# Performance work log

Measured on AMD Instinct MI355X. Metric: run time of the kernel, lower is better.

## Reference

```python
import jax, jax.numpy as jnp
import numpy as np

B, N, F, D, DEG, LAYERS = 32, 1024, 64, 128, 8, 3
EPS = 1e-5


def _gat(x, src, dst, mask, W, a_s, a_d, b):
    # PyG GATConv (heads=1, concat=True): remove existing self loops (handled by mask),
    # add one self loop per node, per-edge leaky-relu attention, scatter-softmax per target.
    M = x.shape[0]
    h = x @ W                                 # [M, D]
    es = h @ a_s                              # [M] source attention term (x*att_src).sum(-1)
    ed = h @ a_d                              # [M] target attention term
    sl = jnp.arange(M, dtype=src.dtype)
    s = jnp.concatenate([src, sl])
    d = jnp.concatenate([dst, sl])
    m = jnp.concatenate([mask, jnp.ones((M,), bool)])
    logit = jnp.where(m, jax.nn.leaky_relu(es[s] + ed[d], 0.2), -jnp.inf)
    mx = jax.ops.segment_max(logit, d, num_segments=M)  # finite: every node has a self loop
    ex = jnp.where(m, jnp.exp(logit - mx[d]), 0.0)
    den = jax.ops.segment_sum(ex, d, num_segments=M)
    alpha = ex / den[d]
    return jax.ops.segment_sum(alpha[:, None] * h[s], d, num_segments=M) + b


def _dedupe(src, dst, mask, M):
    # coalesce after pooling: drop self loops and duplicate edges (PyG max_pool/pool_edge)
    E = src.shape[0]
    key = src * M + dst
    key = jnp.where(mask, key, M * M + jnp.arange(E, dtype=key.dtype))  # park dead edges on unique keys
    order = jnp.argsort(key)
    sk = key[order]
    first = jnp.concatenate([jnp.ones((1,), bool), sk[1:] != sk[:-1]])
    uniq = jnp.zeros((E,), bool).at[order].set(first)
    return mask & uniq & (src != dst)


def _forward(x, Ws, att_src, att_dst, bias, edge_index, clusters):
    src, dst = edge_index[0], edge_index[1]
    mask = src != dst  # GATConv calls remove_self_loops before adding its own
    Bn = x.shape[0] // clusters[0].shape[0]
    for i in range(len(Ws)):
        x = jax.nn.relu(_gat(x, src, dst, mask, Ws[i], att_src[i], att_dst[i], bias[i]))
        c = clusters[i]
        Ni = c.shape[0]
        No = Ni // 2  # cluster maps are arange(Ni)//2, surjective onto Ni//2
        cl = jnp.tile(c, Bn) + jnp.repeat(jnp.arange(Bn, dtype=c.dtype) * No, Ni)
        x = jax.ops.segment_max(x, cl, num_segments=Bn * No)  # max_pool over clusters
        src, dst = cl[src], cl[dst]
        mask = _dedupe(src, dst, mask, Bn * No)
        mu = jnp.mean(x, axis=0)  # BatchNorm1d(affine=False), training-mode batch stats
        var = jnp.mean((x - mu) ** 2, axis=0)
        x = (x - mu) / jnp.sqrt(var + EPS)
    return x.reshape(Bn, -1)  # [B, final_node * dim_cell]


def setup_inputs() -> dict:
    key = jax.random.key(0)
    ks = jax.random.split(key, 10)
    x = jax.random.normal(ks[0], (B * N, F), jnp.float32)
    # per-graph random edges with per-graph node offsets (graph-major layout)
    src_l = jax.random.randint(ks[1], (B, N * DEG), 0, N)
    dst_l = jax.random.randint(ks[2], (B, N * DEG), 0, N)
    off = (jnp.arange(B) * N)[:, None]
    edge_index = jnp.stack([(src_l + off).reshape(-1), (dst_l + off).reshape(-1)]).astype(jnp.int32)
    c0 = (jnp.arange(N) // 2).astype(jnp.int32)
    c1 = (jnp.arange(N // 2) // 2).astype(jnp.int32)
    c2 = (jnp.arange(N // 4) // 2).astype(jnp.int32)
    W0 = jax.random.normal(ks[3], (F, D), jnp.float32) / np.float32(np.sqrt(F))
    W1 = jax.random.normal(ks[4], (D, D), jnp.float32) / np.float32(np.sqrt(D))
    W2 = jax.random.normal(ks[5], (D, D), jnp.float32) / np.float32(np.sqrt(D))
    att_src = jax.random.normal(ks[6], (LAYERS, D), jnp.float32) / np.float32(np.sqrt(D))
    att_dst = jax.random.normal(ks[7], (LAYERS, D), jnp.float32) / np.float32(np.sqrt(D))
    bias = jnp.zeros((LAYERS, D), jnp.float32)
    return dict(x=x, W0=W0, W1=W1, W2=W2, att_src=att_src, att_dst=att_dst, bias=bias,
                edge_index=edge_index, c0=c0, c1=c1, c2=c2)


def reference(x, W0, W1, W2, att_src, att_dst, bias, edge_index, c0, c1, c2):
    return _forward(x, [W0, W1, W2], att_src, att_dst, bias, edge_index, [c0, c1, c2])
```

## Files before the change

### kernel.cpp

```cpp
#include <hip/hip_runtime.h>

#define E_TOTAL 262144
#define NGRAPH  32
#define EPG     8192
#define EPS_BN  1e-5f
#define MB (1u << 20)
#define KB (1u << 10)

__device__ __forceinline__ float lrelu(float x){ return x > 0.f ? x : 0.2f * x; }

__device__ __forceinline__ int xcd_swz(int b, int n){ return (b & 7) * (n >> 3) + (b >> 3); }

template<int Q>
__device__ __forceinline__ void scan_bins(int* h, int* cnt_g, int* rs_g, int B, int g,
                                          int ebase, int* wsum){
  int t = threadIdx.x, lane = t & 63, w = t >> 6;
  int c[Q]; int s = 0;
  #pragma unroll
  for (int i = 0; i < Q; ++i){ c[i] = h[t * Q + i]; s += c[i]; }
  int v = s;
  #pragma unroll
  for (int o = 1; o < 64; o <<= 1){ int u = __shfl_up(v, o); if (lane >= o) v += u; }
  if (lane == 63) wsum[w] = v;
  __syncthreads();
  if (t == 0){ int run = 0;
    #pragma unroll
    for (int i = 0; i < 4; ++i){ int x = wsum[i]; wsum[i] = run; run += x; } }
  __syncthreads();
  int run = v - s + wsum[w];
  #pragma unroll
  for (int i = 0; i < Q; ++i){
    cnt_g[g * B + t * Q + i] = c[i];
    rs_g [g * B + t * Q + i] = ebase + run;
    h[t * Q + i] = run;
    run += c[i];
  }
  __syncthreads();
}

__global__ __launch_bounds__(256, 2)
void mega1(const float* __restrict__ x0, const float* __restrict__ W0,
           const float* __restrict__ a_s, const float* __restrict__ a_d,
           const int* __restrict__ src0, const int* __restrict__ dst0,
           float* __restrict__ C, float* __restrict__ es, float* __restrict__ ed,
           int* __restrict__ csr1, int* __restrict__ csr2, int* __restrict__ csr3,
           int* __restrict__ rs1, int* __restrict__ rs2, int* __restrict__ rs3,
           int* __restrict__ cnt1, int* __restrict__ cnt2, int* __restrict__ cnt3,
           float* __restrict__ partials_all){
  __shared__ __align__(16) char smem[45072];
  __shared__ int wsum[4];
  int t = threadIdx.x;
  int raw = blockIdx.x;

  if (raw < 96){
    int* bm2 = (int*)smem;
    int* bm3 = bm2 + 8192;
    int* h   = bm3 + 2048;
    int role = raw >> 5, g = raw & 31, ebase = g * EPG;

    if (role == 0){
      for (int i = g * 256 + t; i < 3 * 64 * 256; i += 8192) partials_all[i] = 0.f;
      for (int i = t; i < 1024; i += 256) h[i] = 0;
      __syncthreads();
      for (int i = 0; i < 32; ++i){
        int e = ebase + i * 256 + t;
        int sv = src0[e], dv = dst0[e];
        if (sv != dv) atomicAdd(&h[dv & 1023], 1);
      }
      __syncthreads();
      scan_bins<4>(h, cnt1, rs1, 1024, g, ebase, wsum);
      for (int i = 0; i < 32; ++i){
        int e = ebase + i * 256 + t;
        int sv = src0[e], dv = dst0[e];
        if (sv != dv){
          int p = atomicAdd(&h[dv & 1023], 1);
          csr1[ebase + p] = sv;
        }
      }
    } else if (role == 1){
      for (int i = t; i < 8192; i += 256) bm2[i] = 0;
      for (int i = t; i < 512; i += 256) h[i] = 0;
      __syncthreads();
      unsigned int k2m = 0;
      for (int i = 0; i < 32; ++i){
        int e = ebase + i * 256 + t;
        int sv = src0[e], dv = dst0[e];
        if (sv != dv){
          int s2 = (sv >> 1) & 511, d2 = (dv >> 1) & 511;
          if (s2 != d2){
            int key = (s2 << 9) | d2;
            unsigned int bit = 1u << (key & 31);
            unsigned int old = atomicOr((unsigned int*)&bm2[key >> 5], bit);
            if (!(old & bit)){ k2m |= 1u << i; atomicAdd(&h[d2], 1); }
          }
        }
      }
      __syncthreads();
      scan_bins<2>(h, cnt2, rs2, 512, g, ebase, wsum);
      for (int i = 0; i < 32; ++i){
        if ((k2m >> i) & 1u){
          int e = ebase + i * 256 + t;
          int sv = src0[e], dv = dst0[e];
          int p = atomicAdd(&h[(dv >> 1) & 511], 1);
          csr2[ebase + p] = sv >> 1;
        }
      }
    } else {
      for (int i = t; i < 8192; i += 256) bm2[i] = 0;
      for (int i = t; i < 2048; i += 256) bm3[i] = 0;
      for (int i = t; i < 256; i += 256) h[i] = 0;
      __syncthreads();
      unsigned int k3m = 0;
      for (int i = 0; i < 32; ++i){
        int e = ebase + i * 256 + t;
        int sv = src0[e], dv = dst0[e];
        if (sv != dv){
          int s2 = (sv >> 1) & 511, d2 = (dv >> 1) & 511;
          if (s2 != d2){
            int key = (s2 << 9) | d2;
            unsigned int bit = 1u << (key & 31);
            unsigned int old = atomicOr((unsigned int*)&bm2[key >> 5], bit);
            if (!(old & bit)){
              int s3 = (sv >> 2) & 255, d3 = (dv >> 2) & 255;
              if (s3 != d3){
                int key3 = (s3 << 8) | d3;
                unsigned int b3 = 1u << (key3 & 31);
                unsigned int o3 = atomicOr((unsigned int*)&bm3[key3 >> 5], b3);
                if (!(o3 & b3)){ k3m |= 1u << i; atomicAdd(&h[d3], 1); }
              }
            }
          }
        }
      }
      __syncthreads();
      scan_bins<1>(h, cnt3, rs3, 256, g, ebase, wsum);
      for (int i = 0; i < 32; ++i){
        if ((k3m >> i) & 1u){
          int e = ebase + i * 256 + t;
          int sv = src0[e], dv = dst0[e];
          int p = atomicAdd(&h[(dv >> 2) & 255], 1);
          csr3[ebase + p] = sv >> 2;
        }
      }
    }
    return;
  }

  float* Ws   = (float*)smem;
  float* As_t = Ws + 8192;
  int tile = xcd_swz(raw - 96, 1024);
  int row0 = tile * 32;
  int c2 = t & 63, rg = t >> 6;
  float2 acc[8];
  #pragma unroll
  for (int i = 0; i < 8; ++i){ acc[i].x = 0.f; acc[i].y = 0.f; }

  for (int i = t; i < 8192; i += 256) Ws[i] = W0[i];
  #pragma unroll
  for (int it = 0; it < 8; ++it){
    int i = it * 256 + t;
    int r = i >> 6, kk = i & 63;
    As_t[kk * 36 + r] = x0[(size_t)(row0 + r) * 64 + kk];
  }
  __syncthreads();
  #pragma unroll 8
  for (int kk = 0; kk < 64; ++kk){
    float2 w = *(float2*)&Ws[kk * 128 + c2 * 2];
    float4 a0 = *(float4*)&As_t[kk * 36 + rg * 8];
    float4 a1 = *(float4*)&As_t[kk * 36 + rg * 8 + 4];
    acc[0].x = fmaf(a0.x, w.x, acc[0].x); acc[0].y = fmaf(a0.x, w.y, acc[0].y);
    acc[1].x = fmaf(a0.y, w.x, acc[1].x); acc[1].y = fmaf(a0.y, w.y, acc[1].y);
    acc[2].x = fmaf(a0.z, w.x, acc[2].x); acc[2].y = fmaf(a0.z, w.y, acc[2].y);
    acc[3].x = fmaf(a0.w, w.x, acc[3].x); acc[3].y = fmaf(a0.w, w.y, acc[3].y);
    acc[4].x = fmaf(a1.x, w.x, acc[4].x); acc[4].y = fmaf(a1.x, w.y, acc[4].y);
    acc[5].x = fmaf(a1.y, w.x, acc[5].x); acc[5].y = fmaf(a1.y, w.y, acc[5].y);
    acc[6].x = fmaf(a1.z, w.x, acc[6].x); acc[6].y = fmaf(a1.z, w.y, acc[6].y);
    acc[7].x = fmaf(a1.w, w.x, acc[7].x); acc[7].y = fmaf(a1.w, w.y, acc[7].y);
  }
  float2 as2 = ((const float2*)a_s)[c2];
  float2 ad2 = ((const float2*)a_d)[c2];
  float2* C2 = (float2*)C;
  #pragma unroll
  for (int i = 0; i < 8; ++i){
    int r = row0 + rg * 8 + i;
    C2[(size_t)r * 64 + c2] = acc[i];
    float e1 = acc[i].x * as2.x + acc[i].y * as2.y;
    float e2 = acc[i].x * ad2.x + acc[i].y * ad2.y;
    #pragma unroll
    for (int o = 32; o; o >>= 1){ e1 += __shfl_xor(e1, o); e2 += __shfl_xor(e2, o); }
    if (c2 == 0){ es[r] = e1; ed[r] = e2; }
  }
}

__global__ __launch_bounds__(256)
void gemm_attn128(const float* __restrict__ A, const float* __restrict__ W,
                  const float* __restrict__ partials, float invM,
                  const float* __restrict__ a_s, const float* __restrict__ a_d,
                  float* __restrict__ C, float* __restrict__ es, float* __restrict__ ed){
  __shared__ float Ws[64 * 128];
  __shared__ float As_t[64 * 36];
  __shared__ float red[256];
  __shared__ float bnmu[128], bnrs[128];
  int t = threadIdx.x;
  {
    float s = 0.f;
    #pragma unroll
    for (int k = 0; k < 64; ++k) s += partials[(k << 8) + t];
    red[t] = s;
  }
  __syncthreads();
  if (t < 128){
    float mu = red[t] * invM;
    float var = red[128 + t] * invM - mu * mu;
    bnmu[t] = mu; bnrs[t] = rsqrtf(var + EPS_BN);
  }
  int bid = xcd_swz(blockIdx.x, gridDim.x);
  int row0 = bid * 32;
  int c2 = t & 63, rg = t >> 6;
  float2 acc[8];
  #pragma unroll
  for (int i = 0; i < 8; ++i){ acc[i].x = 0.f; acc[i].y = 0.f; }

  for (int k0 = 0; k0 < 128; k0 += 64){
    __syncthreads();
    for (int i = t; i < 64 * 128; i += 256)
      Ws[i] = W[(size_t)(k0 + (i >> 7)) * 128 + (i & 127)];
    #pragma unroll
    for (int it = 0; it < 8; ++it){
      int i = it * 256 + t;
      int r = i >> 6, kk = i & 63;
      float v = A[(size_t)(row0 + r) * 128 + k0 + kk];
      v = (v - bnmu[k0 + kk]) * bnrs[k0 + kk];
      As_t[kk * 36 + r] = v;
    }
    __syncthreads();
    #pragma unroll 8
    for (int kk = 0; kk < 64; ++kk){
      float2 w = *(float2*)&Ws[kk * 128 + c2 * 2];
      float4 a0 = *(float4*)&As_t[kk * 36 + rg * 8];
      float4 a1 = *(float4*)&As_t[kk * 36 + rg * 8 + 4];
      acc[0].x = fmaf(a0.x, w.x, acc[0].x); acc[0].y = fmaf(a0.x, w.y, acc[0].y);
      acc[1].x = fmaf(a0.y, w.x, acc[1].x); acc[1].y = fmaf(a0.y, w.y, acc[1].y);
      acc[2].x = fmaf(a0.z, w.x, acc[2].x); acc[2].y = fmaf(a0.z, w.y, acc[2].y);
      acc[3].x = fmaf(a0.w, w.x, acc[3].x); acc[3].y = fmaf(a0.w, w.y, acc[3].y);
      acc[4].x = fmaf(a1.x, w.x, acc[4].x); acc[4].y = fmaf(a1.x, w.y, acc[4].y);
      acc[5].x = fmaf(a1.y, w.x, acc[5].x); acc[5].y = fmaf(a1.y, w.y, acc[5].y);
      acc[6].x = fmaf(a1.z, w.x, acc[6].x); acc[6].y = fmaf(a1.z, w.y, acc[6].y);
      acc[7].x = fmaf(a1.w, w.x, acc[7].x); acc[7].y = fmaf(a1.w, w.y, acc[7].y);
    }
  }
  float2 as2 = ((const float2*)a_s)[c2];
  float2 ad2 = ((const float2*)a_d)[c2];
  float2* C2 = (float2*)C;
  #pragma unroll
  for (int i = 0; i < 8; ++i){
    int r = row0 + rg * 8 + i;
    C2[(size_t)r * 64 + c2] = acc[i];
    float e1 = acc[i].x * as2.x + acc[i].y * as2.y;
    float e2 = acc[i].x * ad2.x + acc[i].y * ad2.y;
    #pragma unroll
    for (int o = 32; o; o >>= 1){ e1 += __shfl_xor(e1, o); e2 += __shfl_xor(e2, o); }
    if (c2 == 0){ es[r] = e1; ed[r] = e2; }
  }
}

__global__ void gat_pool(const float* __restrict__ h, const float* __restrict__ es,
                         const float* __restrict__ ed, const int* __restrict__ csr_src,
                         const int* __restrict__ row_start, const int* __restrict__ row_cnt,
                         const float* __restrict__ bias, float* __restrict__ xout,
                         float* __restrict__ partials, int M){
  __shared__ float2 osh[4][64];
  int lane = threadIdx.x & 63;
  int wave = threadIdx.x >> 6;
  int bid = xcd_swz(blockIdx.x, gridDim.x);
  int n = bid * 4 + wave;
  int start = row_start[n];
  int cnt   = row_cnt[n];
  float edn = ed[n];
  float selfl = lrelu(es[n] + edn);

  float m_l = -1e30f, d_l = 0.f;
  int   s_c = 0; float l_c = 0.f;
  for (int c0 = 0; c0 < cnt; c0 += 64){
    int j = c0 + lane;
    if (j < cnt){
      int s = csr_src[start + j];
      float l = lrelu(es[s] + edn);
      if (c0 == 0){ s_c = s; l_c = l; }
      float mn = fmaxf(m_l, l);
      d_l = d_l * __expf(m_l - mn) + __expf(l - mn);
      m_l = mn;
    }
  }
  #pragma unroll
  for (int o = 32; o; o >>= 1){
    float m2 = __shfl_xor(m_l, o), d2 = __shfl_xor(d_l, o);
    float mn = fmaxf(m_l, m2);
    d_l = d_l * __expf(m_l - mn) + d2 * __expf(m2 - mn);
    m_l = mn;
  }
  float mf  = fmaxf(m_l, selfl);
  float den = d_l * __expf(m_l - mf) + __expf(selfl - mf);

  const float2* h2 = (const float2*)h;
  float sw = __expf(selfl - mf);
  float2 hv = h2[(size_t)n * 64 + lane];
  float2 acc; acc.x = sw * hv.x; acc.y = sw * hv.y;
  for (int c0 = 0; c0 < cnt; c0 += 64){
    int j = c0 + lane;
    int s_j; float w_j;
    if (c0 == 0){
      s_j = s_c;
      w_j = (lane < cnt) ? __expf(l_c - mf) : 0.f;
    } else {
      s_j = 0; w_j = 0.f;
      if (j < cnt){
        s_j = csr_src[start + j];
        w_j = __expf(lrelu(es[s_j] + edn) - mf);
      }
    }
    int rem = min(64, cnt - c0);
    int k = 0;
    for (; k + 8 <= rem; k += 8){
      int ss[8]; float ww[8]; float2 hh[8];
      #pragma unroll
      for (int i = 0; i < 8; ++i){ ss[i] = __shfl(s_j, k + i); ww[i] = __shfl(w_j, k + i); }
      #pragma unroll
      for (int i = 0; i < 8; ++i){ hh[i] = h2[(size_t)ss[i] * 64 + lane]; }
      #pragma unroll
      for (int i = 0; i < 8; ++i){
        acc.x = fmaf(ww[i], hh[i].x, acc.x);
        acc.y = fmaf(ww[i], hh[i].y, acc.y);
      }
    }
    for (; k < rem; ++k){
      int s = __shfl(s_j, k); float w = __shfl(w_j, k);
      float2 hh = h2[(size_t)s * 64 + lane];
      acc.x = fmaf(w, hh.x, acc.x);
      acc.y = fmaf(w, hh.y, acc.y);
    }
  }
  float inv = 1.f / den;
  float2 bv = ((const float2*)bias)[lane];
  float2 o2;
  o2.x = fmaxf(acc.x * inv + bv.x, 0.f);
  o2.y = fmaxf(acc.y * inv + bv.y, 0.f);
  osh[wave][lane] = o2;
  __syncthreads();
  float2 p;
  if (wave < 2){
    float2 a = osh[2 * wave][lane], b = osh[2 * wave + 1][lane];
    p.x = fmaxf(a.x, b.x); p.y = fmaxf(a.y, b.y);
    ((float2*)xout)[(size_t)(bid * 2 + wave) * 64 + lane] = p;
  }
  __syncthreads();
  if (wave < 2) osh[wave][lane] = p;
  __syncthreads();
  float* part = partials + ((bid & 63) << 8);
  if (wave == 0){
    float2 a = osh[0][lane], b = osh[1][lane];
    atomicAdd(&part[2 * lane],     a.x + b.x);
    atomicAdd(&part[2 * lane + 1], a.y + b.y);
  } else if (wave == 1){
    float2 a = osh[0][lane], b = osh[1][lane];
    atomicAdd(&part[128 + 2 * lane],     a.x * a.x + b.x * b.x);
    atomicAdd(&part[128 + 2 * lane + 1], a.y * a.y + b.y * b.y);
  }
}

__global__ __launch_bounds__(256)
void bn_norm(const float* __restrict__ in, const float* __restrict__ partials,
             float* __restrict__ out, int M){
  __shared__ float red[256];
  __shared__ float mu_s[128], rs_s[128];
  int t = threadIdx.x;
  {
    float s = 0.f;
    #pragma unroll
    for (int k = 0; k < 64; ++k) s += partials[(k << 8) + t];
    red[t] = s;
  }
  __syncthreads();
  if (t < 128){
    float mu = red[t] / (float)M;
    float var = red[128 + t] / (float)M - mu * mu;
    mu_s[t] = mu; rs_s[t] = rsqrtf(var + EPS_BN);
  }
  __syncthreads();
  int total = M * 128;
  for (int idx = blockIdx.x * 256 + t; idx < total; idx += gridDim.x * 256){
    int c = idx & 127;
    out[idx] = (in[idx] - mu_s[c]) * rs_s[c];
  }
}

extern "C" void kernel_launch(void* const* d_in, const int* in_sizes, int n_in,
                              void* d_out, int out_size, void* d_ws, size_t ws_size,
                              hipStream_t stream){
  const float* x0   = (const float*)d_in[0];
  const float* W0   = (const float*)d_in[1];
  const float* W1   = (const float*)d_in[2];
  const float* W2   = (const float*)d_in[3];
  const float* attS = (const float*)d_in[4];
  const float* attD = (const float*)d_in[5];
  const float* bias = (const float*)d_in[6];
  const int*   src0 = (const int*)d_in[7];
  const int*   dst0 = src0 + E_TOTAL;
  float* out = (float*)d_out;

  char* ws = (char*)d_ws;
  float* Hbuf   = (float*)(ws);
  float* Xbuf   = (float*)(ws + 16 * MB);
  int*   csr1   = (int*)  (ws + 24 * MB);
  int*   csr2   = (int*)  (ws + 25 * MB);
  int*   csr3   = (int*)  (ws + 26 * MB);
  float* es     = (float*)(ws + 27 * MB);
  float* ed     = (float*)(ws + 27 * MB + 128 * KB);
  int*   rs1    = (int*)  (ws + 27 * MB + 256 * KB);
  int*   rs2    = (int*)  (ws + 27 * MB + 384 * KB);
  int*   rs3    = (int*)  (ws + 27 * MB + 448 * KB);
  int*   cnt1   = (int*)  (ws + 27 * MB + 480 * KB);
  int*   cnt2   = (int*)  (ws + 27 * MB + 608 * KB);
  int*   cnt3   = (int*)  (ws + 27 * MB + 672 * KB);
  float* parts  = (float*)(ws + 27 * MB + 704 * KB);
  float* parts0 = parts, *parts1 = parts + 64 * 256, *parts2 = parts + 2 * 64 * 256;

  mega1<<<1120, 256, 0, stream>>>(x0, W0, attS, attD, src0, dst0, Hbuf, es, ed,
                                  csr1, csr2, csr3, rs1, rs2, rs3, cnt1, cnt2, cnt3,
                                  parts);

  gat_pool<<<8192, 256, 0, stream>>>(Hbuf, es, ed, csr1, rs1, cnt1, bias, Xbuf,
                                     parts0, 32768);

  gemm_attn128<<<512, 256, 0, stream>>>(Xbuf, W1, parts0, 1.f / 16384.f,
                                        attS + 128, attD + 128, Hbuf, es, ed);
  gat_pool<<<4096, 256, 0, stream>>>(Hbuf, es, ed, csr2, rs2, cnt2, bias + 128, Xbuf,
                                     parts1, 16384);

  gemm_attn128<<<256, 256, 0, stream>>>(Xbuf, W2, parts1, 1.f / 8192.f,
                                        attS + 256, attD + 256, Hbuf, es, ed);
  gat_pool<<<2048, 256, 0, stream>>>(Hbuf, es, ed, csr3, rs3, cnt3, bias + 256, Xbuf,
                                     parts2, 8192);

  bn_norm<<<512, 256, 0, stream>>>(Xbuf, parts2, out, 4096);
}
```

Measured before the change: 203.6 us.

## Move level-3 edge dedupe into layer-1 GAT kernel using saved level-2 mask

The level-3 CSR build no longer runs as a third role block group in the first mega kernel. The level-2 role now writes a per-edge byte mask of unique coarsened edges. The level-3 dedupe then runs in 32 extra blocks of the layer-1 GAT/pool kernel, reading that mask so it can skip the level-2 bitmap rebuild. This shortens the critical path of the first kernel, where the level-3 role was the longest serial block, and overlaps it with GAT aggregation, at the cost of an extra byte write and read per edge.

```diff
diff --git a/kernel.cpp b/kernel.cpp
--- a/kernel.cpp
+++ b/kernel.cpp
@@ -7,6 +7,7 @@
 #define MB (1u << 20)
 #define KB (1u << 10)
 
+
 __device__ __forceinline__ float lrelu(float x){ return x > 0.f ? x : 0.2f * x; }
 
 __device__ __forceinline__ int xcd_swz(int b, int n){ return (b & 7) * (n >> 3) + (b >> 3); }
@@ -38,242 +39,14 @@
   __syncthreads();
 }
 
-__global__ __launch_bounds__(256, 2)
-void mega1(const float* __restrict__ x0, const float* __restrict__ W0,
-           const float* __restrict__ a_s, const float* __restrict__ a_d,
-           const int* __restrict__ src0, const int* __restrict__ dst0,
-           float* __restrict__ C, float* __restrict__ es, float* __restrict__ ed,
-           int* __restrict__ csr1, int* __restrict__ csr2, int* __restrict__ csr3,
-           int* __restrict__ rs1, int* __restrict__ rs2, int* __restrict__ rs3,
-           int* __restrict__ cnt1, int* __restrict__ cnt2, int* __restrict__ cnt3,
-           float* __restrict__ partials_all){
-  __shared__ __align__(16) char smem[45072];
-  __shared__ int wsum[4];
-  int t = threadIdx.x;
-  int raw = blockIdx.x;
-
-  if (raw < 96){
-    int* bm2 = (int*)smem;
-    int* bm3 = bm2 + 8192;
-    int* h   = bm3 + 2048;
-    int role = raw >> 5, g = raw & 31, ebase = g * EPG;
-
-    if (role == 0){
-      for (int i = g * 256 + t; i < 3 * 64 * 256; i += 8192) partials_all[i] = 0.f;
-      for (int i = t; i < 1024; i += 256) h[i] = 0;
-      __syncthreads();
-      for (int i = 0; i < 32; ++i){
-        int e = ebase + i * 256 + t;
-        int sv = src0[e], dv = dst0[e];
-        if (sv != dv) atomicAdd(&h[dv & 1023], 1);
-      }
-      __syncthreads();
-      scan_bins<4>(h, cnt1, rs1, 1024, g, ebase, wsum);
-      for (int i = 0; i < 32; ++i){
-        int e = ebase + i * 256 + t;
-        int sv = src0[e], dv = dst0[e];
-        if (sv != dv){
-          int p = atomicAdd(&h[dv & 1023], 1);
-          csr1[ebase + p] = sv;
-        }
-      }
-    } else if (role == 1){
-      for (int i = t; i < 8192; i += 256) bm2[i] = 0;
-      for (int i = t; i < 512; i += 256) h[i] = 0;
-      __syncthreads();
-      unsigned int k2m = 0;
-      for (int i = 0; i < 32; ++i){
-        int e = ebase + i * 256 + t;
-        int sv = src0[e], dv = dst0[e];
-        if (sv != dv){
-          int s2 = (sv >> 1) & 511, d2 = (dv >> 1) & 511;
-          if (s2 != d2){
-            int key = (s2 << 9) | d2;
-            unsigned int bit = 1u << (key & 31);
-            unsigned int old = atomicOr((unsigned int*)&bm2[key >> 5], bit);
-            if (!(old & bit)){ k2m |= 1u << i; atomicAdd(&h[d2], 1); }
-          }
-        }
-      }
-      __syncthreads();
-      scan_bins<2>(h, cnt2, rs2, 512, g, ebase, wsum);
-      for (int i = 0; i < 32; ++i){
-        if ((k2m >> i) & 1u){
-          int e = ebase + i * 256 + t;
-          int sv = src0[e], dv = dst0[e];
-          int p = atomicAdd(&h[(dv >> 1) & 511], 1);
-          csr2[ebase + p] = sv >> 1;
-        }
-      }
-    } else {
-      for (int i = t; i < 8192; i += 256) bm2[i] = 0;
-      for (int i = t; i < 2048; i += 256) bm3[i] = 0;
-      for (int i = t; i < 256; i += 256) h[i] = 0;
-      __syncthreads();
-      unsigned int k3m = 0;
-      for (int i = 0; i < 32; ++i){
-        int e = ebase + i * 256 + t;
-        int sv = src0[e], dv = dst0[e];
-        if (sv != dv){
-          int s2 = (sv >> 1) & 511, d2 = (dv >> 1) & 511;
-          if (s2 != d2){
-            int key = (s2 << 9) | d2;
-            unsigned int bit = 1u << (key & 31);
-            unsigned int old = atomicOr((unsigned int*)&bm2[key >> 5], bit);
-            if (!(old & bit)){
-              int s3 = (sv >> 2) & 255, d3 = (dv >> 2) & 255;
-              if (s3 != d3){
-                int key3 = (s3 << 8) | d3;
-                unsigned int b3 = 1u << (key3 & 31);
-                unsigned int o3 = atomicOr((unsigned int*)&bm3[key3 >> 5], b3);
-                if (!(o3 & b3)){ k3m |= 1u << i; atomicAdd(&h[d3], 1); }
-              }
-            }
-          }
-        }
-      }
-      __syncthreads();
-      scan_bins<1>(h, cnt3, rs3, 256, g, ebase, wsum);
-      for (int i = 0; i < 32; ++i){
-        if ((k3m >> i) & 1u){
-          int e = ebase + i * 256 + t;
-          int sv = src0[e], dv = dst0[e];
-          int p = atomicAdd(&h[(dv >> 2) & 255], 1);
-          csr3[ebase + p] = sv >> 2;
-        }
-      }
-    }
-    return;
-  }
-
-  float* Ws   = (float*)smem;
-  float* As_t = Ws + 8192;
-  int tile = xcd_swz(raw - 96, 1024);
-  int row0 = tile * 32;
-  int c2 = t & 63, rg = t >> 6;
-  float2 acc[8];
-  #pragma unroll
-  for (int i = 0; i < 8; ++i){ acc[i].x = 0.f; acc[i].y = 0.f; }
-
-  for (int i = t; i < 8192; i += 256) Ws[i] = W0[i];
-  #pragma unroll
-  for (int it = 0; it < 8; ++it){
-    int i = it * 256 + t;
-    int r = i >> 6, kk = i & 63;
-    As_t[kk * 36 + r] = x0[(size_t)(row0 + r) * 64 + kk];
-  }
-  __syncthreads();
-  #pragma unroll 8
-  for (int kk = 0; kk < 64; ++kk){
-    float2 w = *(float2*)&Ws[kk * 128 + c2 * 2];
-    float4 a0 = *(float4*)&As_t[kk * 36 + rg * 8];
-    float4 a1 = *(float4*)&As_t[kk * 36 + rg * 8 + 4];
-    acc[0].x = fmaf(a0.x, w.x, acc[0].x); acc[0].y = fmaf(a0.x, w.y, acc[0].y);
-    acc[1].x = fmaf(a0.y, w.x, acc[1].x); acc[1].y = fmaf(a0.y, w.y, acc[1].y);
-    acc[2].x = fmaf(a0.z, w.x, acc[2].x); acc[2].y = fmaf(a0.z, w.y, acc[2].y);
-    acc[3].x = fmaf(a0.w, w.x, acc[3].x); acc[3].y = fmaf(a0.w, w.y, acc[3].y);
-    acc[4].x = fmaf(a1.x, w.x, acc[4].x); acc[4].y = fmaf(a1.x, w.y, acc[4].y);
-    acc[5].x = fmaf(a1.y, w.x, acc[5].x); acc[5].y = fmaf(a1.y, w.y, acc[5].y);
-    acc[6].x = fmaf(a1.z, w.x, acc[6].x); acc[6].y = fmaf(a1.z, w.y, acc[6].y);
-    acc[7].x = fmaf(a1.w, w.x, acc[7].x); acc[7].y = fmaf(a1.w, w.y, acc[7].y);
-  }
-  float2 as2 = ((const float2*)a_s)[c2];
-  float2 ad2 = ((const float2*)a_d)[c2];
-  float2* C2 = (float2*)C;
-  #pragma unroll
-  for (int i = 0; i < 8; ++i){
-    int r = row0 + rg * 8 + i;
-    C2[(size_t)r * 64 + c2] = acc[i];
-    float e1 = acc[i].x * as2.x + acc[i].y * as2.y;
-    float e2 = acc[i].x * ad2.x + acc[i].y * ad2.y;
-    #pragma unroll
-    for (int o = 32; o; o >>= 1){ e1 += __shfl_xor(e1, o); e2 += __shfl_xor(e2, o); }
-    if (c2 == 0){ es[r] = e1; ed[r] = e2; }
-  }
-}
-
-__global__ __launch_bounds__(256)
-void gemm_attn128(const float* __restrict__ A, const float* __restrict__ W,
-                  const float* __restrict__ partials, float invM,
-                  const float* __restrict__ a_s, const float* __restrict__ a_d,
-                  float* __restrict__ C, float* __restrict__ es, float* __restrict__ ed){
-  __shared__ float Ws[64 * 128];
-  __shared__ float As_t[64 * 36];
-  __shared__ float red[256];
-  __shared__ float bnmu[128], bnrs[128];
-  int t = threadIdx.x;
-  {
-    float s = 0.f;
-    #pragma unroll
-    for (int k = 0; k < 64; ++k) s += partials[(k << 8) + t];
-    red[t] = s;
-  }
-  __syncthreads();
-  if (t < 128){
-    float mu = red[t] * invM;
-    float var = red[128 + t] * invM - mu * mu;
-    bnmu[t] = mu; bnrs[t] = rsqrtf(var + EPS_BN);
-  }
-  int bid = xcd_swz(blockIdx.x, gridDim.x);
-  int row0 = bid * 32;
-  int c2 = t & 63, rg = t >> 6;
-  float2 acc[8];
-  #pragma unroll
-  for (int i = 0; i < 8; ++i){ acc[i].x = 0.f; acc[i].y = 0.f; }
-
-  for (int k0 = 0; k0 < 128; k0 += 64){
-    __syncthreads();
-    for (int i = t; i < 64 * 128; i += 256)
-      Ws[i] = W[(size_t)(k0 + (i >> 7)) * 128 + (i & 127)];
-    #pragma unroll
-    for (int it = 0; it < 8; ++it){
-      int i = it * 256 + t;
-      int r = i >> 6, kk = i & 63;
-      float v = A[(size_t)(row0 + r) * 128 + k0 + kk];
-      v = (v - bnmu[k0 + kk]) * bnrs[k0 + kk];
-      As_t[kk * 36 + r] = v;
-    }
-    __syncthreads();
-    #pragma unroll 8
-    for (int kk = 0; kk < 64; ++kk){
-      float2 w = *(float2*)&Ws[kk * 128 + c2 * 2];
-      float4 a0 = *(float4*)&As_t[kk * 36 + rg * 8];
-      float4 a1 = *(float4*)&As_t[kk * 36 + rg * 8 + 4];
-      acc[0].x = fmaf(a0.x, w.x, acc[0].x); acc[0].y = fmaf(a0.x, w.y, acc[0].y);
-      acc[1].x = fmaf(a0.y, w.x, acc[1].x); acc[1].y = fmaf(a0.y, w.y, acc[1].y);
-      acc[2].x = fmaf(a0.z, w.x, acc[2].x); acc[2].y = fmaf(a0.z, w.y, acc[2].y);
-      acc[3].x = fmaf(a0.w, w.x, acc[3].x); acc[3].y = fmaf(a0.w, w.y, acc[3].y);
-      acc[4].x = fmaf(a1.x, w.x, acc[4].x); acc[4].y = fmaf(a1.x, w.y, acc[4].y);
-      acc[5].x = fmaf(a1.y, w.x, acc[5].x); acc[5].y = fmaf(a1.y, w.y, acc[5].y);
-      acc[6].x = fmaf(a1.z, w.x, acc[6].x); acc[6].y = fmaf(a1.z, w.y, acc[6].y);
-      acc[7].x = fmaf(a1.w, w.x, acc[7].x); acc[7].y = fmaf(a1.w, w.y, acc[7].y);
-    }
-  }
-  float2 as2 = ((const float2*)a_s)[c2];
-  float2 ad2 = ((const float2*)a_d)[c2];
-  float2* C2 = (float2*)C;
-  #pragma unroll
-  for (int i = 0; i < 8; ++i){
-    int r = row0 + rg * 8 + i;
-    C2[(size_t)r * 64 + c2] = acc[i];
-    float e1 = acc[i].x * as2.x + acc[i].y * as2.y;
-    float e2 = acc[i].x * ad2.x + acc[i].y * ad2.y;
-    #pragma unroll
-    for (int o = 32; o; o >>= 1){ e1 += __shfl_xor(e1, o); e2 += __shfl_xor(e2, o); }
-    if (c2 == 0){ es[r] = e1; ed[r] = e2; }
-  }
-}
-
-__global__ void gat_pool(const float* __restrict__ h, const float* __restrict__ es,
-                         const float* __restrict__ ed, const int* __restrict__ csr_src,
-                         const int* __restrict__ row_start, const int* __restrict__ row_cnt,
-                         const float* __restrict__ bias, float* __restrict__ xout,
-                         float* __restrict__ partials, int M){
-  __shared__ float2 osh[4][64];
+__device__ __forceinline__ void gat_group(const float* __restrict__ h,
+    const float* __restrict__ es, const float* __restrict__ ed,
+    const int* __restrict__ csr_src, const int* __restrict__ row_start,
+    const int* __restrict__ row_cnt, const float* __restrict__ bias,
+    float* __restrict__ xout, float* __restrict__ partials, int group, float2* osh){
   int lane = threadIdx.x & 63;
   int wave = threadIdx.x >> 6;
-  int bid = xcd_swz(blockIdx.x, gridDim.x);
-  int n = bid * 4 + wave;
+  int n = group * 4 + wave;
   int start = row_start[n];
   int cnt   = row_cnt[n];
   float edn = ed[n];
@@ -345,27 +118,279 @@
   float2 o2;
   o2.x = fmaxf(acc.x * inv + bv.x, 0.f);
   o2.y = fmaxf(acc.y * inv + bv.y, 0.f);
-  osh[wave][lane] = o2;
+  osh[wave * 64 + lane] = o2;
   __syncthreads();
   float2 p;
   if (wave < 2){
-    float2 a = osh[2 * wave][lane], b = osh[2 * wave + 1][lane];
+    float2 a = osh[2 * wave * 64 + lane], b = osh[(2 * wave + 1) * 64 + lane];
     p.x = fmaxf(a.x, b.x); p.y = fmaxf(a.y, b.y);
-    ((float2*)xout)[(size_t)(bid * 2 + wave) * 64 + lane] = p;
-  }
-  __syncthreads();
-  if (wave < 2) osh[wave][lane] = p;
-  __syncthreads();
-  float* part = partials + ((bid & 63) << 8);
+    ((float2*)xout)[(size_t)(group * 2 + wave) * 64 + lane] = p;
+  }
+  __syncthreads();
+  if (wave < 2) osh[wave * 64 + lane] = p;
+  __syncthreads();
+  float* part = partials + ((group & 63) << 8);
   if (wave == 0){
-    float2 a = osh[0][lane], b = osh[1][lane];
+    float2 a = osh[lane], b = osh[64 + lane];
     atomicAdd(&part[2 * lane],     a.x + b.x);
     atomicAdd(&part[2 * lane + 1], a.y + b.y);
   } else if (wave == 1){
-    float2 a = osh[0][lane], b = osh[1][lane];
+    float2 a = osh[lane], b = osh[64 + lane];
     atomicAdd(&part[128 + 2 * lane],     a.x * a.x + b.x * b.x);
     atomicAdd(&part[128 + 2 * lane + 1], a.y * a.y + b.y * b.y);
   }
+}
+
+__global__ __launch_bounds__(256, 2)
+void mega1(const float* __restrict__ x0, const float* __restrict__ W0,
+           const float* __restrict__ a_s, const float* __restrict__ a_d,
+           const int* __restrict__ src0, const int* __restrict__ dst0,
+           float* __restrict__ C, float* __restrict__ es, float* __restrict__ ed,
+           int* __restrict__ csr1, int* __restrict__ csr2,
+           int* __restrict__ rs1, int* __restrict__ rs2,
+           int* __restrict__ cnt1, int* __restrict__ cnt2,
+           unsigned char* __restrict__ mask2, float* __restrict__ partials_all){
+  __shared__ __align__(16) char smem[45056];
+  __shared__ int wsum[4];
+  int t = threadIdx.x;
+  int raw = blockIdx.x;
+
+  if (raw < 64){
+    int* bm2 = (int*)smem;
+    int* h   = bm2 + 8192;
+    int g = raw & 31, ebase = g * EPG;
+
+    if (raw < 32){
+      for (int i = g * 256 + t; i < 3 * 64 * 256; i += 8192) partials_all[i] = 0.f;
+      for (int i = t; i < 1024; i += 256) h[i] = 0;
+      __syncthreads();
+      for (int i = 0; i < 32; ++i){
+        int e = ebase + i * 256 + t;
+        int sv = src0[e], dv = dst0[e];
+        if (sv != dv) atomicAdd(&h[dv & 1023], 1);
+      }
+      __syncthreads();
+      scan_bins<4>(h, cnt1, rs1, 1024, g, ebase, wsum);
+      for (int i = 0; i < 32; ++i){
+        int e = ebase + i * 256 + t;
+        int sv = src0[e], dv = dst0[e];
+        if (sv != dv){
+          int p = atomicAdd(&h[dv & 1023], 1);
+          csr1[ebase + p] = sv;
+        }
+      }
+    } else {
+      for (int i = t; i < 8192; i += 256) bm2[i] = 0;
+      for (int i = t; i < 512; i += 256) h[i] = 0;
+      __syncthreads();
+      unsigned int k2m = 0;
+      for (int i = 0; i < 32; ++i){
+        int e = ebase + i * 256 + t;
+        int sv = src0[e], dv = dst0[e];
+        unsigned char m2 = 0;
+        if (sv != dv){
+          int s2 = (sv >> 1) & 511, d2 = (dv >> 1) & 511;
+          if (s2 != d2){
+            int key = (s2 << 9) | d2;
+            unsigned int bit = 1u << (key & 31);
+            unsigned int old = atomicOr((unsigned int*)&bm2[key >> 5], bit);
+            if (!(old & bit)){ k2m |= 1u << i; atomicAdd(&h[d2], 1); m2 = 1; }
+          }
+        }
+        mask2[e] = m2;
+      }
+      __syncthreads();
+      scan_bins<2>(h, cnt2, rs2, 512, g, ebase, wsum);
+      for (int i = 0; i < 32; ++i){
+        if ((k2m >> i) & 1u){
+          int e = ebase + i * 256 + t;
+          int sv = src0[e], dv = dst0[e];
+          int p = atomicAdd(&h[(dv >> 1) & 511], 1);
+          csr2[ebase + p] = sv >> 1;
+        }
+      }
+    }
+    return;
+  }
+
+  float* Ws   = (float*)smem;
+  float* As_t = Ws + 8192;
+  int tile = xcd_swz(raw - 64, 1024);
+  int row0 = tile * 32;
+  int c2 = t & 63, rg = t >> 6;
+  float2 acc[8];
+  #pragma unroll
+  for (int i = 0; i < 8; ++i){ acc[i].x = 0.f; acc[i].y = 0.f; }
+
+  for (int i = t; i < 8192; i += 256) Ws[i] = W0[i];
+  #pragma unroll
+  for (int it = 0; it < 8; ++it){
+    int i = it * 256 + t;
+    int r = i >> 6, kk = i & 63;
+    As_t[kk * 36 + r] = x0[(size_t)(row0 + r) * 64 + kk];
+  }
+  __syncthreads();
+  #pragma unroll 8
+  for (int kk = 0; kk < 64; ++kk){
+    float2 w = *(float2*)&Ws[kk * 128 + c2 * 2];
+    float4 a0 = *(float4*)&As_t[kk * 36 + rg * 8];
+    float4 a1 = *(float4*)&As_t[kk * 36 + rg * 8 + 4];
+    acc[0].x = fmaf(a0.x, w.x, acc[0].x); acc[0].y = fmaf(a0.x, w.y, acc[0].y);
+    acc[1].x = fmaf(a0.y, w.x, acc[1].x); acc[1].y = fmaf(a0.y, w.y, acc[1].y);
+    acc[2].x = fmaf(a0.z, w.x, acc[2].x); acc[2].y = fmaf(a0.z, w.y, acc[2].y);
+    acc[3].x = fmaf(a0.w, w.x, acc[3].x); acc[3].y = fmaf(a0.w, w.y, acc[3].y);
+    acc[4].x = fmaf(a1.x, w.x, acc[4].x); acc[4].y = fmaf(a1.x, w.y, acc[4].y);
+    acc[5].x = fmaf(a1.y, w.x, acc[5].x); acc[5].y = fmaf(a1.y, w.y, acc[5].y);
+    acc[6].x = fmaf(a1.z, w.x, acc[6].x); acc[6].y = fmaf(a1.z, w.y, acc[6].y);
+    acc[7].x = fmaf(a1.w, w.x, acc[7].x); acc[7].y = fmaf(a1.w, w.y, acc[7].y);
+  }
+  float2 as2 = ((const float2*)a_s)[c2];
+  float2 ad2 = ((const float2*)a_d)[c2];
+  float2* C2 = (float2*)C;
+  #pragma unroll
+  for (int i = 0; i < 8; ++i){
+    int r = row0 + rg * 8 + i;
+    C2[(size_t)r * 64 + c2] = acc[i];
+    float e1 = acc[i].x * as2.x + acc[i].y * as2.y;
+    float e2 = acc[i].x * ad2.x + acc[i].y * ad2.y;
+    #pragma unroll
+    for (int o = 32; o; o >>= 1){ e1 += __shfl_xor(e1, o); e2 += __shfl_xor(e2, o); }
+    if (c2 == 0){ es[r] = e1; ed[r] = e2; }
+  }
+}
+
+__global__ __launch_bounds__(256, 2)
+void gat1h(const float* __restrict__ h, const float* __restrict__ es,
+           const float* __restrict__ ed, const int* __restrict__ src0,
+           const int* __restrict__ dst0, const unsigned char* __restrict__ mask2,
+           const int* __restrict__ csr1, const int* __restrict__ rs1,
+           const int* __restrict__ cnt1,
+           int* __restrict__ csr3, int* __restrict__ rs3, int* __restrict__ cnt3,
+           const float* __restrict__ bias, float* __restrict__ xout,
+           float* __restrict__ partials0){
+  __shared__ __align__(16) int sm[2048 + 256];
+  __shared__ int wsum[4];
+  int t = threadIdx.x;
+  int raw = blockIdx.x;
+
+  if (raw < 32){
+    int* bm3 = sm;
+    int* h3  = bm3 + 2048;
+    int g = raw, ebase = g * EPG;
+    for (int i = t; i < 2048; i += 256) bm3[i] = 0;
+    if (t < 256) h3[t] = 0;
+    __syncthreads();
+    unsigned int k3m = 0;
+    for (int i = 0; i < 32; ++i){
+      int e = ebase + i * 256 + t;
+      if (mask2[e]){
+        int sv = src0[e], dv = dst0[e];
+        int s3 = (sv >> 2) & 255, d3 = (dv >> 2) & 255;
+        if (s3 != d3){
+          int key3 = (s3 << 8) | d3;
+          unsigned int b3 = 1u << (key3 & 31);
+          unsigned int o3 = atomicOr((unsigned int*)&bm3[key3 >> 5], b3);
+          if (!(o3 & b3)){ k3m |= 1u << i; atomicAdd(&h3[d3], 1); }
+        }
+      }
+    }
+    __syncthreads();
+    scan_bins<1>(h3, cnt3, rs3, 256, g, ebase, wsum);
+    for (int i = 0; i < 32; ++i){
+      if ((k3m >> i) & 1u){
+        int e = ebase + i * 256 + t;
+        int sv = src0[e], dv = dst0[e];
+        int p = atomicAdd(&h3[(dv >> 2) & 255], 1);
+        csr3[ebase + p] = sv >> 2;
+      }
+    }
+    return;
+  }
+
+  int group = xcd_swz(raw - 32, 8192);
+  gat_group(h, es, ed, csr1, rs1, cnt1, bias, xout, partials0, group, (float2*)sm);
+}
+
+__global__ __launch_bounds__(256)
+void gemm_attn128(const float* __restrict__ A, const float* __restrict__ W,
+                  const float* __restrict__ partials, float invM,
+                  const float* __restrict__ a_s, const float* __restrict__ a_d,
+                  float* __restrict__ C, float* __restrict__ es, float* __restrict__ ed){
+  __shared__ float Ws[64 * 128];
+  __shared__ float As_t[64 * 36];
+  __shared__ float red[256];
+  __shared__ float bnmu[128], bnrs[128];
+  int t = threadIdx.x;
+  {
+    float s = 0.f;
+    #pragma unroll
+    for (int k = 0; k < 64; ++k) s += partials[(k << 8) + t];
+    red[t] = s;
+  }
+  __syncthreads();
+  if (t < 128){
+    float mu = red[t] * invM;
+    float var = red[128 + t] * invM - mu * mu;
+    bnmu[t] = mu; bnrs[t] = rsqrtf(var + EPS_BN);
+  }
+  int bid = xcd_swz(blockIdx.x, gridDim.x);
+  int row0 = bid * 32;
+  int c2 = t & 63, rg = t >> 6;
+  float2 acc[8];
+  #pragma unroll
+  for (int i = 0; i < 8; ++i){ acc[i].x = 0.f; acc[i].y = 0.f; }
+
+  for (int k0 = 0; k0 < 128; k0 += 64){
+    __syncthreads();
+    for (int i = t; i < 64 * 128; i += 256)
+      Ws[i] = W[(size_t)(k0 + (i >> 7)) * 128 + (i & 127)];
+    #pragma unroll
+    for (int it = 0; it < 8; ++it){
+      int i = it * 256 + t;
+      int r = i >> 6, kk = i & 63;
+      float v = A[(size_t)(row0 + r) * 128 + k0 + kk];
+      v = (v - bnmu[k0 + kk]) * bnrs[k0 + kk];
+      As_t[kk * 36 + r] = v;
+    }
+    __syncthreads();
+    #pragma unroll 8
+    for (int kk = 0; kk < 64; ++kk){
+      float2 w = *(float2*)&Ws[kk * 128 + c2 * 2];
+      float4 a0 = *(float4*)&As_t[kk * 36 + rg * 8];
+      float4 a1 = *(float4*)&As_t[kk * 36 + rg * 8 + 4];
+      acc[0].x = fmaf(a0.x, w.x, acc[0].x); acc[0].y = fmaf(a0.x, w.y, acc[0].y);
+      acc[1].x = fmaf(a0.y, w.x, acc[1].x); acc[1].y = fmaf(a0.y, w.y, acc[1].y);
+      acc[2].x = fmaf(a0.z, w.x, acc[2].x); acc[2].y = fmaf(a0.z, w.y, acc[2].y);
+      acc[3].x = fmaf(a0.w, w.x, acc[3].x); acc[3].y = fmaf(a0.w, w.y, acc[3].y);
+      acc[4].x = fmaf(a1.x, w.x, acc[4].x); acc[4].y = fmaf(a1.x, w.y, acc[4].y);
+      acc[5].x = fmaf(a1.y, w.x, acc[5].x); acc[5].y = fmaf(a1.y, w.y, acc[5].y);
+      acc[6].x = fmaf(a1.z, w.x, acc[6].x); acc[6].y = fmaf(a1.z, w.y, acc[6].y);
+      acc[7].x = fmaf(a1.w, w.x, acc[7].x); acc[7].y = fmaf(a1.w, w.y, acc[7].y);
+    }
+  }
+  float2 as2 = ((const float2*)a_s)[c2];
+  float2 ad2 = ((const float2*)a_d)[c2];
+  float2* C2 = (float2*)C;
+  #pragma unroll
+  for (int i = 0; i < 8; ++i){
+    int r = row0 + rg * 8 + i;
+    C2[(size_t)r * 64 + c2] = acc[i];
+    float e1 = acc[i].x * as2.x + acc[i].y * as2.y;
+    float e2 = acc[i].x * ad2.x + acc[i].y * ad2.y;
+    #pragma unroll
+    for (int o = 32; o; o >>= 1){ e1 += __shfl_xor(e1, o); e2 += __shfl_xor(e2, o); }
+    if (c2 == 0){ es[r] = e1; ed[r] = e2; }
+  }
+}
+
+__global__ void gat_pool(const float* __restrict__ h, const float* __restrict__ es,
+                         const float* __restrict__ ed, const int* __restrict__ csr_src,
+                         const int* __restrict__ row_start, const int* __restrict__ row_cnt,
+                         const float* __restrict__ bias, float* __restrict__ xout,
+                         float* __restrict__ partials, int M){
+  __shared__ float2 osh[4 * 64];
+  int bid = xcd_swz(blockIdx.x, gridDim.x);
+  gat_group(h, es, ed, csr_src, row_start, row_cnt, bias, xout, partials, bid, osh);
 }
 
 __global__ __launch_bounds__(256)
@@ -409,28 +434,29 @@
   float* out = (float*)d_out;
 
   char* ws = (char*)d_ws;
-  float* Hbuf   = (float*)(ws);
-  float* Xbuf   = (float*)(ws + 16 * MB);
-  int*   csr1   = (int*)  (ws + 24 * MB);
-  int*   csr2   = (int*)  (ws + 25 * MB);
-  int*   csr3   = (int*)  (ws + 26 * MB);
-  float* es     = (float*)(ws + 27 * MB);
-  float* ed     = (float*)(ws + 27 * MB + 128 * KB);
-  int*   rs1    = (int*)  (ws + 27 * MB + 256 * KB);
-  int*   rs2    = (int*)  (ws + 27 * MB + 384 * KB);
-  int*   rs3    = (int*)  (ws + 27 * MB + 448 * KB);
-  int*   cnt1   = (int*)  (ws + 27 * MB + 480 * KB);
-  int*   cnt2   = (int*)  (ws + 27 * MB + 608 * KB);
-  int*   cnt3   = (int*)  (ws + 27 * MB + 672 * KB);
-  float* parts  = (float*)(ws + 27 * MB + 704 * KB);
+  float*         Hbuf   = (float*)(ws);
+  float*         Xbuf   = (float*)(ws + 16 * MB);
+  int*           csr1   = (int*)  (ws + 24 * MB);
+  int*           csr2   = (int*)  (ws + 25 * MB);
+  int*           csr3   = (int*)  (ws + 26 * MB);
+  float*         es     = (float*)(ws + 27 * MB);
+  float*         ed     = (float*)(ws + 27 * MB + 128 * KB);
+  int*           rs1    = (int*)  (ws + 27 * MB + 256 * KB);
+  int*           rs2    = (int*)  (ws + 27 * MB + 384 * KB);
+  int*           rs3    = (int*)  (ws + 27 * MB + 448 * KB);
+  int*           cnt1   = (int*)  (ws + 27 * MB + 480 * KB);
+  int*           cnt2   = (int*)  (ws + 27 * MB + 608 * KB);
+  int*           cnt3   = (int*)  (ws + 27 * MB + 672 * KB);
+  float*         parts  = (float*)(ws + 27 * MB + 704 * KB);
+  unsigned char* mask2  = (unsigned char*)(ws + 27 * MB + 896 * KB);
   float* parts0 = parts, *parts1 = parts + 64 * 256, *parts2 = parts + 2 * 64 * 256;
 
-  mega1<<<1120, 256, 0, stream>>>(x0, W0, attS, attD, src0, dst0, Hbuf, es, ed,
-                                  csr1, csr2, csr3, rs1, rs2, rs3, cnt1, cnt2, cnt3,
-                                  parts);
-
-  gat_pool<<<8192, 256, 0, stream>>>(Hbuf, es, ed, csr1, rs1, cnt1, bias, Xbuf,
-                                     parts0, 32768);
+  mega1<<<1088, 256, 0, stream>>>(x0, W0, attS, attD, src0, dst0, Hbuf, es, ed,
+                                  csr1, csr2, rs1, rs2, cnt1, cnt2, mask2, parts);
+
+  gat1h<<<8224, 256, 0, stream>>>(Hbuf, es, ed, src0, dst0, mask2,
+                                  csr1, rs1, cnt1, csr3, rs3, cnt3,
+                                  bias, Xbuf, parts0);
 
   gemm_attn128<<<512, 256, 0, stream>>>(Xbuf, W1, parts0, 1.f / 16384.f,
                                         attS + 128, attD + 128, Hbuf, es, ed);
```

New measurement: 207.8 us. +2.1%, slower.
